# Kernel optimization log

Measured on AMD Instinct MI355X. Metric: run time of the kernel, lower is better.

The kernel has to match this reference:

```python
import jax, jax.numpy as jnp
import numpy as np

TAU = 2.0        # LIF membrane time constant
VTH = 1.0        # spike threshold
VRESET = 0.0     # hard reset voltage
ALPHA = 2.0      # ATan surrogate alpha
LN_EPS = 1e-5


@jax.custom_vjp
def atan_spike(x):
    # Heaviside forward, ATan surrogate backward (spikingjelly surrogate.ATan)
    return (x >= 0.0).astype(x.dtype)

def _atan_fwd(x):
    return atan_spike(x), x

def _atan_bwd(x, g):
    z = (jnp.pi / 2.0) * ALPHA * x
    return (g * (ALPHA / 2.0) / (1.0 + z * z),)

atan_spike.defvjp(_atan_fwd, _atan_bwd)


def layer_norm(x, w, b):
    mu = jnp.mean(x, axis=-1, keepdims=True)
    var = jnp.mean(jnp.square(x - mu), axis=-1, keepdims=True)
    return (x - mu) * jax.lax.rsqrt(var + LN_EPS) * w + b


def time_shift(x):
    # x: [B,T,C] -> x shifted by one step in time, zero-padded at t=0
    return jnp.pad(x, ((0, 0), (1, 0), (0, 0)))[:, :-1]


def wkv(time_decay, time_first, k, v):
    # Numerically-stable RWKV WKV recurrence. k, v: [B,T,C]
    w = -jnp.exp(time_decay)  # [C]
    u = time_first            # [C]
    B, T, C = k.shape
    kT = jnp.moveaxis(k, 1, 0)  # [T,B,C]
    vT = jnp.moveaxis(v, 1, 0)
    init = (jnp.zeros((B, C), k.dtype),
            jnp.zeros((B, C), k.dtype),
            jnp.full((B, C), -1e38, k.dtype))

    def step(carry, kv_t):
        aa, bb, pp = carry
        kt, vt = kv_t
        ww = u + kt
        p = jnp.maximum(pp, ww)
        e1 = jnp.exp(pp - p)
        e2 = jnp.exp(ww - p)
        y = (e1 * aa + e2 * vt) / (e1 * bb + e2)
        ww2 = pp + w
        p2 = jnp.maximum(ww2, kt)
        e1b = jnp.exp(ww2 - p2)
        e2b = jnp.exp(kt - p2)
        return (e1b * aa + e2b * vt, e1b * bb + e2b, p2), y

    _, yT = jax.lax.scan(step, init, (kT, vT))
    return jnp.moveaxis(yT, 0, 1)  # [B,T,C]


def lif(x):
    # MultiStepLIFNode: tau=2, decay_input=True, v_th=1, hard reset to 0.
    # Recurrence runs over the sequence dim (permute(1,0,2) in torch is layout only).
    xT = jnp.moveaxis(x, 1, 0)  # [T,B,C]
    v0 = jnp.zeros_like(xT[0])

    def step(v, xt):
        v = v + (xt - (v - VRESET)) / TAU
        s = atan_spike(v - VTH)
        v = (1.0 - s) * v + s * VRESET
        return v, s

    _, sT = jax.lax.scan(step, v0, xT)
    return jnp.moveaxis(sT, 0, 1)


def rwkv_time_mix(x, time_decay, time_first, mix_k, mix_v, mix_r, Wk, Wv, Wr, Wo):
    xx = time_shift(x)
    xk = x * mix_k + xx * (1.0 - mix_k)
    xv = x * mix_v + xx * (1.0 - mix_v)
    xr = x * mix_r + xx * (1.0 - mix_r)
    k = jnp.einsum('btc,cd->btd', xk, Wk)
    v = jnp.einsum('btc,cd->btd', xv, Wv)
    r = jax.nn.sigmoid(jnp.einsum('btc,cd->btd', xr, Wr))
    y = wkv(time_decay, time_first, k, v)
    return jnp.einsum('btc,cd->btd', r * y, Wo)


def rwkv_channel_mix(x, mix_k, mix_r, Wk, Wv, Wr):
    xx = time_shift(x)
    xk = x * mix_k + xx * (1.0 - mix_k)
    xr = x * mix_r + xx * (1.0 - mix_r)
    k = jnp.square(jax.nn.relu(jnp.einsum('btc,ch->bth', xk, Wk)))  # relu^2
    kv = jnp.einsum('bth,hc->btc', k, Wv)
    return jax.nn.sigmoid(jnp.einsum('btc,cd->btd', xr, Wr)) * kv


def setup_inputs() -> dict:
    key = jax.random.key(0)
    B, T, C, H = 8, 2048, 768, 3072
    ks = jax.random.split(key, 20)
    p = lambda k, shape, s=0.02: (jax.random.normal(k, shape, jnp.float32) * s)
    u = lambda k, shape: jax.random.uniform(k, shape, jnp.float32)
    return {
        'x': jax.random.normal(ks[0], (B, T, C), jnp.float32),
        'ln1_w': jnp.ones((C,), jnp.float32), 'ln1_b': jnp.zeros((C,), jnp.float32),
        'ln2_w': jnp.ones((C,), jnp.float32), 'ln2_b': jnp.zeros((C,), jnp.float32),
        'att_time_decay': p(ks[1], (C,), 1.0),
        'att_time_first': p(ks[2], (C,), 1.0),
        'att_mix_k': u(ks[3], (C,)), 'att_mix_v': u(ks[4], (C,)), 'att_mix_r': u(ks[5], (C,)),
        'att_Wk': p(ks[6], (C, C)), 'att_Wv': p(ks[7], (C, C)),
        'att_Wr': p(ks[8], (C, C)), 'att_Wo': p(ks[9], (C, C)),
        'ffn_mix_k': u(ks[10], (C,)), 'ffn_mix_r': u(ks[11], (C,)),
        'ffn_Wk': p(ks[12], (C, H)), 'ffn_Wv': p(ks[13], (H, C)), 'ffn_Wr': p(ks[14], (C, C)),
    }


def reference(x, ln1_w, ln1_b, ln2_w, ln2_b,
              att_time_decay, att_time_first, att_mix_k, att_mix_v, att_mix_r,
              att_Wk, att_Wv, att_Wr, att_Wo,
              ffn_mix_k, ffn_mix_r, ffn_Wk, ffn_Wv, ffn_Wr):
    # Block.forward with layer_id != 0 (no ln0, att path); dropout in eval mode.
    a = rwkv_time_mix(layer_norm(x, ln1_w, ln1_b), att_time_decay, att_time_first,
                      att_mix_k, att_mix_v, att_mix_r, att_Wk, att_Wv, att_Wr, att_Wo)
    x = x + lif(a)
    f = rwkv_channel_mix(layer_norm(x, ln2_w, ln2_b), ffn_mix_k, ffn_mix_r,
                         ffn_Wk, ffn_Wv, ffn_Wr)
    x = x + lif(f)
    return x
```

## Files before the change

kernel.cpp:

```cpp
#include <hip/hip_runtime.h>

#define B_ 8
#define T_ 2048
#define C_ 768
#define H_ 3072
#define BT_ (B_ * T_)
#define BC_ (B_ * C_)
#define WSEG 128
#define NWSEG 16
#define LSEG 128
#define NLSEG 16
#define LWARM 96

typedef unsigned short u16;
typedef short bf16x8 __attribute__((ext_vector_type(8)));
typedef float f32x4 __attribute__((ext_vector_type(4)));

__device__ __forceinline__ float b2f(u16 u) {
    union { unsigned i; float f; } w; w.i = ((unsigned)u) << 16; return w.f;
}
__device__ __forceinline__ u16 f2b(float f) {
    union { float f; unsigned i; } w; w.f = f;
    return (u16)((w.i + 0x7fffu + ((w.i >> 16) & 1u)) >> 16);
}

typedef __attribute__((address_space(3))) unsigned int lds_u32;
typedef const __attribute__((address_space(1))) unsigned int glb_u32;
__device__ __forceinline__ void gld_lds16(const void* g, void* l) {
    __builtin_amdgcn_global_load_lds((glb_u32*)g, (lds_u32*)l, 16, 0, 0);
}

template<int NOUT>
__global__ void lnmix(const float* __restrict__ x, const float* __restrict__ w,
                      const float* __restrict__ b,
                      const float* __restrict__ m1, const float* __restrict__ m2,
                      const float* __restrict__ m3,
                      u16* __restrict__ o1, u16* __restrict__ o2, u16* __restrict__ o3) {
    int row = blockIdx.x;
    int t = row % T_;
    const float* xr = x + (size_t)row * C_;
    const float* xp = xr - C_;
    int tid = threadIdx.x;
    float s = 0.f, s2 = 0.f, ps = 0.f, ps2 = 0.f;
    for (int i = tid; i < C_; i += 256) {
        float v = xr[i]; s += v; s2 += v * v;
        if (t > 0) { float u = xp[i]; ps += u; ps2 += u * u; }
    }
    for (int off = 32; off > 0; off >>= 1) {
        s += __shfl_down(s, off);  s2 += __shfl_down(s2, off);
        ps += __shfl_down(ps, off); ps2 += __shfl_down(ps2, off);
    }
    __shared__ float red[4][4];
    int wid = tid >> 6, lane = tid & 63;
    if (lane == 0) { red[wid][0] = s; red[wid][1] = s2; red[wid][2] = ps; red[wid][3] = ps2; }
    __syncthreads();
    if (tid == 0) {
        float a0 = 0, a1 = 0, a2 = 0, a3 = 0;
        for (int i = 0; i < 4; ++i) { a0 += red[i][0]; a1 += red[i][1]; a2 += red[i][2]; a3 += red[i][3]; }
        red[0][0] = a0; red[0][1] = a1; red[0][2] = a2; red[0][3] = a3;
    }
    __syncthreads();
    float mu = red[0][0] * (1.f / C_);
    float rs = rsqrtf(red[0][1] * (1.f / C_) - mu * mu + 1e-5f);
    float pmu = red[0][2] * (1.f / C_);
    float prs = rsqrtf(red[0][3] * (1.f / C_) - pmu * pmu + 1e-5f);
    size_t ob = (size_t)row * C_;
    for (int i = tid; i < C_; i += 256) {
        float wi = w[i], bi = b[i];
        float n = (xr[i] - mu) * rs * wi + bi;
        float np = (t > 0) ? (xp[i] - pmu) * prs * wi + bi : 0.f;
        o1[ob + i] = f2b(fmaf(m1[i], n - np, np));
        o2[ob + i] = f2b(fmaf(m2[i], n - np, np));
        if constexpr (NOUT == 3) o3[ob + i] = f2b(fmaf(m3[i], n - np, np));
    }
}

struct TCJ { const float* s; u16* d; int R, Ncol, nbx, b0; };
struct TC7 { TCJ j[7]; };
__global__ void tcast_all(TC7 jobs) {
    __shared__ float t[32][33];
    int bid = blockIdx.x;
    int ji = 0;
#pragma unroll
    for (int k = 1; k < 7; ++k) if (bid >= jobs.j[k].b0) ji = k;
    TCJ jb = jobs.j[ji];
    int local = bid - jb.b0;
    int bx = local % jb.nbx, by = local / jb.nbx;
    int c0 = bx * 32, r0 = by * 32;
    int col = threadIdx.x & 31, rw = threadIdx.x >> 5;
#pragma unroll
    for (int i = 0; i < 4; ++i) {
        int r = rw + i * 8;
        t[r][col] = jb.s[(size_t)(r0 + r) * jb.Ncol + c0 + col];
    }
    __syncthreads();
#pragma unroll
    for (int i = 0; i < 4; ++i) {
        int r = rw + i * 8;
        jb.d[(size_t)(c0 + r) * jb.R + r0 + col] = f2b(t[col][r]);
    }
}

__device__ __forceinline__ void gemm_core256(const u16* __restrict__ A,
                                             const u16* __restrict__ WT,
                                             int K, int m0, int n0,
                                             u16* L, f32x4 acc[8][4]) {
    const int tid = threadIdx.x;
    const int lane = tid & 63, wid = tid >> 6;
    const int wr = wid >> 2, wc = wid & 3;
    const int r16 = lane & 15, g = lane >> 4;

    const int srow = tid >> 3;
    const int sunit = tid & 7;
    const int ssw = sunit ^ (srow & 7);
    const u16* gA = A + (size_t)(m0 + srow) * K + ssw * 8;
    const u16* gB = WT + (size_t)(n0 + srow) * K + ssw * 8;
    u16* lA = L + tid * 8;
    u16* lB = L + 16384 + tid * 8;

#define STGA(buf) do { \
        gld_lds16(gA,                   lA + (buf) * 32768); \
        gld_lds16(gA + (size_t)64 * K,  lA + (buf) * 32768 + 4096); \
        gld_lds16(gA + (size_t)128 * K, lA + (buf) * 32768 + 8192); \
        gld_lds16(gA + (size_t)192 * K, lA + (buf) * 32768 + 12288); \
        gA += 64; } while (0)
#define STGB(buf) do { \
        gld_lds16(gB,                   lB + (buf) * 32768); \
        gld_lds16(gB + (size_t)64 * K,  lB + (buf) * 32768 + 4096); \
        gld_lds16(gB + (size_t)128 * K, lB + (buf) * 32768 + 8192); \
        gld_lds16(gB + (size_t)192 * K, lB + (buf) * 32768 + 12288); \
        gB += 64; } while (0)

    int offA[8], offB[4];
#pragma unroll
    for (int m = 0; m < 8; ++m) {
        int row = wr * 128 + m * 16 + r16;
        offA[m] = row * 64 + (g ^ (row & 7)) * 8;
    }
#pragma unroll
    for (int n = 0; n < 4; ++n) {
        int rob = wc * 64 + n * 16 + r16;
        offB[n] = 16384 + rob * 64 + (g ^ (rob & 7)) * 8;
    }

    const int nt = K >> 6;
    STGA(0); STGB(0);
    asm volatile("s_waitcnt vmcnt(0)" ::: "memory");
    __builtin_amdgcn_sched_barrier(0);
    __builtin_amdgcn_s_barrier();

    for (int t = 0; t < nt; ++t) {
        const u16* Lb = L + (t & 1) * 32768;
        const bool stg = (t + 1 < nt);
        bf16x8 a0[8], b0[4];
#pragma unroll
        for (int m = 0; m < 8; ++m) a0[m] = *(const bf16x8*)(Lb + offA[m]);
#pragma unroll
        for (int n = 0; n < 4; ++n) b0[n] = *(const bf16x8*)(Lb + offB[n]);
        __builtin_amdgcn_sched_barrier(0);
        if (stg) { STGA((t + 1) & 1); STGB((t + 1) & 1); }
        asm volatile("s_waitcnt lgkmcnt(0)" ::: "memory");
        __builtin_amdgcn_sched_barrier(0);
        __builtin_amdgcn_s_setprio(1);
#pragma unroll
        for (int m = 0; m < 8; ++m)
#pragma unroll
            for (int n = 0; n < 4; ++n)
                acc[m][n] = __builtin_amdgcn_mfma_f32_16x16x32_bf16(a0[m], b0[n], acc[m][n], 0, 0, 0);
        __builtin_amdgcn_s_setprio(0);
        __builtin_amdgcn_sched_barrier(0);
        bf16x8 a1[8], b1[4];
#pragma unroll
        for (int m = 0; m < 8; ++m) a1[m] = *(const bf16x8*)(Lb + (offA[m] ^ 32));
#pragma unroll
        for (int n = 0; n < 4; ++n) b1[n] = *(const bf16x8*)(Lb + (offB[n] ^ 32));
        asm volatile("s_waitcnt lgkmcnt(0)" ::: "memory");
        __builtin_amdgcn_sched_barrier(0);
        __builtin_amdgcn_s_setprio(1);
#pragma unroll
        for (int m = 0; m < 8; ++m)
#pragma unroll
            for (int n = 0; n < 4; ++n)
                acc[m][n] = __builtin_amdgcn_mfma_f32_16x16x32_bf16(a1[m], b1[n], acc[m][n], 0, 0, 0);
        __builtin_amdgcn_s_setprio(0);
        __builtin_amdgcn_sched_barrier(0);
        if (stg) {
            asm volatile("s_waitcnt vmcnt(0)" ::: "memory");
            __builtin_amdgcn_sched_barrier(0);
            __builtin_amdgcn_s_barrier();
        }
    }
#undef STGA
#undef STGB
}

__device__ __forceinline__ void xcd_remap2(int& bx, int& by) {
    const int gx = gridDim.x;
    const int nwg = gx * gridDim.y;
    const int lin = blockIdx.y * gx + blockIdx.x;
    const int q = nwg >> 3, r = nwg & 7;
    const int xcd = lin & 7, pos = lin >> 3;
    const int nid = (xcd < r ? xcd * (q + 1) : r * (q + 1) + (xcd - r) * q) + pos;
    const int g4 = gx << 2;
    const int grp = nid / g4, rem = nid - grp * g4;
    by = (grp << 2) + (rem & 3);
    bx = rem >> 2;
}

__device__ __forceinline__ void epilogue256(f32x4 acc[8][4], u16* O, const u16* Emul,
                                            int m0, int n0, int N, int mode, bool emul) {
    const int lane = threadIdx.x & 63, wid = threadIdx.x >> 6;
    const int wr = wid >> 2, wc = wid & 3;
    const int r16 = lane & 15, g = lane >> 4;
#pragma unroll
    for (int m = 0; m < 8; ++m)
#pragma unroll
        for (int n = 0; n < 4; ++n)
#pragma unroll
            for (int j = 0; j < 4; ++j) {
                int row = m0 + wr * 128 + m * 16 + g * 4 + j;
                int col = n0 + wc * 64 + n * 16 + r16;
                float v = acc[m][n][j];
                if (mode == 1) v = 1.f / (1.f + expf(-v));
                else if (mode == 2) { v = fmaxf(v, 0.f); v = v * v; }
                size_t o = (size_t)row * N + col;
                if (emul) v *= b2f(Emul[o]);
                O[o] = f2b(v);
            }
}

template<int MODE, bool EMUL>
__global__ __launch_bounds__(512, 1)
void gemm256(const u16* __restrict__ A, const u16* __restrict__ WT,
             u16* __restrict__ Cout, const u16* __restrict__ Emul, int N, int K) {
    __shared__ u16 L[65536];
    int bx, by;
    xcd_remap2(bx, by);
    const int m0 = by << 8, n0 = bx << 8;
    f32x4 acc[8][4];
#pragma unroll
    for (int i = 0; i < 8; ++i)
#pragma unroll
        for (int j = 0; j < 4; ++j)
#pragma unroll
            for (int q = 0; q < 4; ++q) acc[i][j][q] = 0.f;
    gemm_core256(A, WT, K, m0, n0, L, acc);
    epilogue256(acc, Cout, Emul, m0, n0, N, MODE, EMUL);
}

struct P3 {
    const u16 *A0, *A1, *A2;
    const u16 *W0, *W1, *W2;
    u16 *O0, *O1, *O2;
};
__global__ __launch_bounds__(512, 1)
void proj3(P3 p, int N, int K) {
    __shared__ u16 L[65536];
    const int z = blockIdx.z;
    const u16* A = (z == 0) ? p.A0 : (z == 1) ? p.A1 : p.A2;
    const u16* W = (z == 0) ? p.W0 : (z == 1) ? p.W1 : p.W2;
    u16* O = (z == 0) ? p.O0 : (z == 1) ? p.O1 : p.O2;
    int bx, by;
    xcd_remap2(bx, by);
    const int m0 = by << 8, n0 = bx << 8;
    f32x4 acc[8][4];
#pragma unroll
    for (int i = 0; i < 8; ++i)
#pragma unroll
        for (int j = 0; j < 4; ++j)
#pragma unroll
            for (int q = 0; q < 4; ++q) acc[i][j][q] = 0.f;
    gemm_core256(A, W, K, m0, n0, L, acc);
    epilogue256(acc, O, nullptr, m0, n0, N, (z == 2) ? 1 : 0, false);
}

struct J2 {
    const u16 *A0, *W0; u16 *O0;
    const u16 *A1, *W1; u16 *O1;
};
__global__ __launch_bounds__(512, 1)
void ffn1rr(J2 p, int K) {
    __shared__ u16 L[65536];
    int bx, by;
    xcd_remap2(bx, by);
    const bool isF = (bx < 12);
    const u16* A = isF ? p.A0 : p.A1;
    const u16* W = isF ? p.W0 : p.W1;
    u16* O = isF ? p.O0 : p.O1;
    const int N = isF ? 3072 : 768;
    const int m0 = by << 8;
    const int n0 = (isF ? bx : bx - 12) << 8;
    f32x4 acc[8][4];
#pragma unroll
    for (int i = 0; i < 8; ++i)
#pragma unroll
        for (int j = 0; j < 4; ++j)
#pragma unroll
            for (int q = 0; q < 4; ++q) acc[i][j][q] = 0.f;
    gemm_core256(A, W, K, m0, n0, L, acc);
    epilogue256(acc, O, nullptr, m0, n0, N, isF ? 2 : 1, false);
}

__global__ void wkv_p1(const float* __restrict__ td, const u16* __restrict__ K,
                       const u16* __restrict__ V, float* __restrict__ st) {
    int bc = blockIdx.x * 256 + threadIdx.x;
    int seg = blockIdx.y;
    int b = bc / C_, c = bc - b * C_;
    float w = -expf(td[c]);
    size_t off = (size_t)b * T_ * C_ + (size_t)seg * WSEG * C_ + c;
    float aa = 0.f, bb = 0.f, pp = -1e38f;
#pragma unroll 4
    for (int i = 0; i < WSEG; ++i) {
        float kt = b2f(K[off + (size_t)i * C_]);
        float vt = b2f(V[off + (size_t)i * C_]);
        float ww2 = pp + w;
        float p2 = fmaxf(ww2, kt);
        float e1 = expf(ww2 - p2);
        float e2 = expf(kt - p2);
        aa = e1 * aa + e2 * vt;
        bb = e1 * bb + e2;
        pp = p2;
    }
    int sidx = seg * 3 * BC_ + bc;
    st[sidx] = aa; st[sidx + BC_] = bb; st[sidx + 2 * BC_] = pp;
}

__global__ void wkv_p3(const float* __restrict__ td, const float* __restrict__ tf,
                       const u16* __restrict__ K, const u16* __restrict__ V,
                       const u16* __restrict__ R, const float* __restrict__ st,
                       u16* __restrict__ RY) {
    int bc = blockIdx.x * 256 + threadIdx.x;
    int seg = blockIdx.y;
    int b = bc / C_, c = bc - b * C_;
    float w = -expf(td[c]);
    float u = tf[c];
    float wL = w * (float)WSEG;
    float aa = 0.f, bb = 0.f, pp = -1e38f;
    for (int s = 0; s < seg; ++s) {
        int sidx = s * 3 * BC_ + bc;
        float la = st[sidx], lb = st[sidx + BC_], lp = st[sidx + 2 * BC_];
        float ppw = pp + wL;
        float p = fmaxf(ppw, lp);
        float e1 = expf(ppw - p), e2 = expf(lp - p);
        aa = e1 * aa + e2 * la;
        bb = e1 * bb + e2 * lb;
        pp = p;
    }
    size_t off = (size_t)b * T_ * C_ + (size_t)seg * WSEG * C_ + c;
#pragma unroll 4
    for (int i = 0; i < WSEG; ++i) {
        float kt = b2f(K[off + (size_t)i * C_]);
        float vt = b2f(V[off + (size_t)i * C_]);
        float rr = b2f(R[off + (size_t)i * C_]);
        float ww = u + kt;
        float p = fmaxf(pp, ww);
        float e1 = expf(pp - p);
        float e2 = expf(ww - p);
        RY[off + (size_t)i * C_] = f2b(rr * (e1 * aa + e2 * vt) / (e1 * bb + e2));
        float ww2 = pp + w;
        float p2 = fmaxf(ww2, kt);
        float e1b = expf(ww2 - p2);
        float e2b = expf(kt - p2);
        aa = e1b * aa + e2b * vt;
        bb = e1b * bb + e2b;
        pp = p2;
    }
}

__global__ void lif_add_b(const u16* __restrict__ cur, const float* __restrict__ base,
                          float* __restrict__ out) {
    int bc = blockIdx.x * 256 + threadIdx.x;
    int seg = blockIdx.y;
    int b = bc / C_, c = bc - b * C_;
    size_t rowbase = (size_t)b * T_ * C_ + c;
    int t0 = seg * LSEG;
    int tw = t0 - LWARM; if (tw < 0) tw = 0;
    int nw = t0 - tw;
    float v = 0.f;
    const u16* cp = cur + rowbase + (size_t)tw * C_;
#pragma unroll 8
    for (int i = 0; i < nw; ++i) {
        float xt = b2f(cp[(size_t)i * C_]);
        v += (xt - v) * 0.5f;
        v = (v >= 1.f) ? 0.f : v;
    }
    const u16* c2 = cur + rowbase + (size_t)t0 * C_;
    const float* bp = base + rowbase + (size_t)t0 * C_;
    float* op = out + rowbase + (size_t)t0 * C_;
#pragma unroll 8
    for (int i = 0; i < LSEG; ++i) {
        float xt = b2f(c2[(size_t)i * C_]);
        v += (xt - v) * 0.5f;
        float sp = (v >= 1.f) ? 1.f : 0.f;
        op[(size_t)i * C_] = bp[(size_t)i * C_] + sp;
        v = (sp > 0.f) ? 0.f : v;
    }
}

extern "C" void kernel_launch(void* const* d_in, const int* in_sizes, int n_in,
                              void* d_out, int out_size, void* d_ws, size_t ws_size,
                              hipStream_t stream) {
    const float* x    = (const float*)d_in[0];
    const float* ln1w = (const float*)d_in[1];
    const float* ln1b = (const float*)d_in[2];
    const float* ln2w = (const float*)d_in[3];
    const float* ln2b = (const float*)d_in[4];
    const float* td   = (const float*)d_in[5];
    const float* tf   = (const float*)d_in[6];
    const float* amk  = (const float*)d_in[7];
    const float* amv  = (const float*)d_in[8];
    const float* amr  = (const float*)d_in[9];
    const float* aWk  = (const float*)d_in[10];
    const float* aWv  = (const float*)d_in[11];
    const float* aWr  = (const float*)d_in[12];
    const float* aWo  = (const float*)d_in[13];
    const float* fmk  = (const float*)d_in[14];
    const float* fmr  = (const float*)d_in[15];
    const float* fWk  = (const float*)d_in[16];
    const float* fWv  = (const float*)d_in[17];
    const float* fWr  = (const float*)d_in[18];
    float* out = (float*)d_out;

    const size_t NBC = (size_t)BT_ * C_;
    u16* WkT = (u16*)d_ws;
    u16* WvT = WkT + 589824;
    u16* WrT = WvT + 589824;
    u16* WoT = WrT + 589824;
    u16* FrT = WoT + 589824;
    u16* FkT = FrT + 589824;
    u16* FvT = FkT + 2359296;
    float* st  = (float*)(FvT + 2359296);
    u16* S0 = (u16*)(st + NWSEG * 3 * BC_);
    u16* S1 = S0 + NBC;
    u16* S2 = S1 + NBC;
    u16* S3 = S2 + NBC;
    u16* Hbuf = S3 + NBC;
    size_t fixed_b = (size_t)((char*)Hbuf - (char*)d_ws);

    int NCH = 4;
    if (ws_size >= fixed_b + ((size_t)BT_ * H_ + NBC) * 2) NCH = 1;
    else if (ws_size >= fixed_b + ((size_t)(BT_ / 2) * H_ + NBC / 2) * 2) NCH = 2;
    const int CH = BT_ / NCH;
    u16* Fbuf = Hbuf + (size_t)CH * H_;

    u16* Kb = (u16*)d_out;
    u16* Vb = Kb + NBC;

    {
        TC7 jobs;
        const float* srcs[7] = {aWk, aWv, aWr, aWo, fWr, fWk, fWv};
        u16* dsts[7] = {WkT, WvT, WrT, WoT, FrT, FkT, FvT};
        int Rs[7]    = {768, 768, 768, 768, 768, 768, 3072};
        int Ns[7]    = {768, 768, 768, 768, 768, 3072, 768};
        int b0 = 0;
        for (int k = 0; k < 7; ++k) {
            jobs.j[k].s = srcs[k]; jobs.j[k].d = dsts[k];
            jobs.j[k].R = Rs[k]; jobs.j[k].Ncol = Ns[k];
            jobs.j[k].nbx = Ns[k] / 32; jobs.j[k].b0 = b0;
            b0 += (Ns[k] / 32) * (Rs[k] / 32);
        }
        tcast_all<<<b0, 256, 0, stream>>>(jobs);
    }

    lnmix<3><<<BT_, 256, 0, stream>>>(x, ln1w, ln1b, amk, amv, amr, S0, S1, S2);
    {
        P3 p{S0, S1, S2, WkT, WvT, WrT, Kb, Vb, S3};
        proj3<<<dim3(3, 64, 3), 512, 0, stream>>>(p, C_, C_);
    }
    wkv_p1<<<dim3(BC_ / 256, NWSEG), 256, 0, stream>>>(td, Kb, Vb, st);
    wkv_p3<<<dim3(BC_ / 256, NWSEG), 256, 0, stream>>>(td, tf, Kb, Vb, S3, st, S0);
    gemm256<0, false><<<dim3(3, 64), 512, 0, stream>>>(S0, WoT, S1, nullptr, C_, C_);
    lif_add_b<<<dim3(BC_ / 256, NLSEG), 256, 0, stream>>>(S1, x, out);
    lnmix<2><<<BT_, 256, 0, stream>>>(out, ln2w, ln2b, fmk, fmr, nullptr, S0, S1, nullptr);

    if (NCH == 1) {
        J2 p{S0, FkT, Hbuf, S1, FrT, S2};
        ffn1rr<<<dim3(15, 64), 512, 0, stream>>>(p, C_);
        gemm256<0, true><<<dim3(3, 64), 512, 0, stream>>>(Hbuf, FvT, Fbuf, S2, C_, H_);
        lif_add_b<<<dim3(BC_ / 256, NLSEG), 256, 0, stream>>>(Fbuf, out, out);
    } else {
        gemm256<1, false><<<dim3(3, 64), 512, 0, stream>>>(S1, FrT, S2, nullptr, C_, C_);
        for (int ch = 0; ch < NCH; ++ch) {
            const u16* xk2c = S0 + (size_t)ch * CH * C_;
            const u16* rrc  = S2 + (size_t)ch * CH * C_;
            gemm256<2, false><<<dim3(12, CH / 256), 512, 0, stream>>>(xk2c, FkT, Hbuf, nullptr, H_, C_);
            gemm256<0, true><<<dim3(3, CH / 256), 512, 0, stream>>>(Hbuf, FvT, Fbuf, rrc, C_, H_);
            lif_add_b<<<dim3((CH / T_) * C_ / 256, NLSEG), 256, 0, stream>>>(
                Fbuf, out + (size_t)ch * CH * C_, out + (size_t)ch * CH * C_);
        }
    }
}
```

Baseline: 563.9 us.

## Restructure 256x256 GEMM main loop into eight-phase quadrant ping-pong pipeline

```diff
diff --git a/kernel.cpp b/kernel.cpp
--- a/kernel.cpp
+++ b/kernel.cpp
@@ -112,86 +112,124 @@
 
     const int srow = tid >> 3;
     const int sunit = tid & 7;
-    const int ssw = sunit ^ (srow & 7);
-    const u16* gA = A + (size_t)(m0 + srow) * K + ssw * 8;
-    const u16* gB = WT + (size_t)(n0 + srow) * K + ssw * 8;
-    u16* lA = L + tid * 8;
-    u16* lB = L + 16384 + tid * 8;
-
-#define STGA(buf) do { \
-        gld_lds16(gA,                   lA + (buf) * 32768); \
-        gld_lds16(gA + (size_t)64 * K,  lA + (buf) * 32768 + 4096); \
-        gld_lds16(gA + (size_t)128 * K, lA + (buf) * 32768 + 8192); \
-        gld_lds16(gA + (size_t)192 * K, lA + (buf) * 32768 + 12288); \
-        gA += 64; } while (0)
-#define STGB(buf) do { \
-        gld_lds16(gB,                   lB + (buf) * 32768); \
-        gld_lds16(gB + (size_t)64 * K,  lB + (buf) * 32768 + 4096); \
-        gld_lds16(gB + (size_t)128 * K, lB + (buf) * 32768 + 8192); \
-        gld_lds16(gB + (size_t)192 * K, lB + (buf) * 32768 + 12288); \
-        gB += 64; } while (0)
+    const u16* pa = A + (size_t)(m0 + srow) * K + ((sunit ^ (srow & 7)) << 3);
+    const u16* pb = WT + (size_t)(n0 + srow) * K + ((sunit ^ (srow & 7)) << 3);
+    u16* lbase = L + tid * 8;
+
+#define STG_A(d, h) do { \
+        const u16* gp = pa + (size_t)((h) ? 128 : 0) * K; \
+        u16* lp = lbase + ((d) * 2 + (h)) * 8192; \
+        gld_lds16(gp, lp); gld_lds16(gp + (size_t)64 * K, lp + 4096); } while (0)
+#define STG_B(d, h) do { \
+        const u16* gp = pb + (size_t)((h) ? 128 : 0) * K; \
+        u16* lp = lbase + 32768 + ((d) * 2 + (h)) * 8192; \
+        gld_lds16(gp, lp); gld_lds16(gp + (size_t)64 * K, lp + 4096); } while (0)
 
     int offA[8], offB[4];
 #pragma unroll
     for (int m = 0; m < 8; ++m) {
-        int row = wr * 128 + m * 16 + r16;
-        offA[m] = row * 64 + (g ^ (row & 7)) * 8;
+        int lr = m * 16 + r16;
+        offA[m] = wr * 8192 + lr * 64 + ((g ^ (lr & 7)) << 3);
     }
 #pragma unroll
     for (int n = 0; n < 4; ++n) {
-        int rob = wc * 64 + n * 16 + r16;
-        offB[n] = 16384 + rob * 64 + (g ^ (rob & 7)) * 8;
-    }
+        int lrb = (wc & 1) * 64 + n * 16 + r16;
+        offB[n] = 32768 + (wc >> 1) * 8192 + lrb * 64 + ((g ^ (lrb & 7)) << 3);
+    }
+
+    bf16x8 aq[4][2], bq[2][2];
+
+#define RD_A(QM, DOFF) do { _Pragma("unroll") \
+        for (int mm = 0; mm < 4; ++mm) { \
+            int o = offA[(QM) * 4 + mm] + (DOFF); \
+            aq[mm][0] = *(const bf16x8*)(L + o); \
+            aq[mm][1] = *(const bf16x8*)(L + (o ^ 32)); } } while (0)
+#define RD_B(QN, DOFF) do { _Pragma("unroll") \
+        for (int nn = 0; nn < 2; ++nn) { \
+            int o = offB[(QN) * 2 + nn] + (DOFF); \
+            bq[nn][0] = *(const bf16x8*)(L + o); \
+            bq[nn][1] = *(const bf16x8*)(L + (o ^ 32)); } } while (0)
+#define MM16(QM, QN) do { _Pragma("unroll") \
+        for (int mm = 0; mm < 4; ++mm) { _Pragma("unroll") \
+            for (int nn = 0; nn < 2; ++nn) { \
+                acc[(QM)*4+mm][(QN)*2+nn] = __builtin_amdgcn_mfma_f32_16x16x32_bf16(aq[mm][0], bq[nn][0], acc[(QM)*4+mm][(QN)*2+nn], 0, 0, 0); \
+                acc[(QM)*4+mm][(QN)*2+nn] = __builtin_amdgcn_mfma_f32_16x16x32_bf16(aq[mm][1], bq[nn][1], acc[(QM)*4+mm][(QN)*2+nn], 0, 0, 0); } } } while (0)
+
+#define PH_MID(MMSTMT) \
+        __builtin_amdgcn_s_barrier(); \
+        asm volatile("s_waitcnt lgkmcnt(0)" ::: "memory"); \
+        __builtin_amdgcn_sched_barrier(0); \
+        __builtin_amdgcn_s_setprio(1); \
+        MMSTMT; \
+        __builtin_amdgcn_s_setprio(0); \
+        __builtin_amdgcn_sched_barrier(0);
 
     const int nt = K >> 6;
-    STGA(0); STGB(0);
-    asm volatile("s_waitcnt vmcnt(0)" ::: "memory");
+    const int nIter = nt >> 1;
+    STG_A(0, 0); STG_A(0, 1); pa += 64;
+    STG_B(0, 0); STG_B(0, 1); pb += 64;
+    STG_A(1, 0); STG_A(1, 1); pa += 64;
+    STG_B(1, 0);
+    asm volatile("s_waitcnt vmcnt(6)" ::: "memory");
     __builtin_amdgcn_sched_barrier(0);
     __builtin_amdgcn_s_barrier();
 
-    for (int t = 0; t < nt; ++t) {
-        const u16* Lb = L + (t & 1) * 32768;
-        const bool stg = (t + 1 < nt);
-        bf16x8 a0[8], b0[4];
-#pragma unroll
-        for (int m = 0; m < 8; ++m) a0[m] = *(const bf16x8*)(Lb + offA[m]);
-#pragma unroll
-        for (int n = 0; n < 4; ++n) b0[n] = *(const bf16x8*)(Lb + offB[n]);
-        __builtin_amdgcn_sched_barrier(0);
-        if (stg) { STGA((t + 1) & 1); STGB((t + 1) & 1); }
-        asm volatile("s_waitcnt lgkmcnt(0)" ::: "memory");
-        __builtin_amdgcn_sched_barrier(0);
-        __builtin_amdgcn_s_setprio(1);
-#pragma unroll
-        for (int m = 0; m < 8; ++m)
-#pragma unroll
-            for (int n = 0; n < 4; ++n)
-                acc[m][n] = __builtin_amdgcn_mfma_f32_16x16x32_bf16(a0[m], b0[n], acc[m][n], 0, 0, 0);
-        __builtin_amdgcn_s_setprio(0);
-        __builtin_amdgcn_sched_barrier(0);
-        bf16x8 a1[8], b1[4];
-#pragma unroll
-        for (int m = 0; m < 8; ++m) a1[m] = *(const bf16x8*)(Lb + (offA[m] ^ 32));
-#pragma unroll
-        for (int n = 0; n < 4; ++n) b1[n] = *(const bf16x8*)(Lb + (offB[n] ^ 32));
-        asm volatile("s_waitcnt lgkmcnt(0)" ::: "memory");
-        __builtin_amdgcn_sched_barrier(0);
-        __builtin_amdgcn_s_setprio(1);
-#pragma unroll
-        for (int m = 0; m < 8; ++m)
-#pragma unroll
-            for (int n = 0; n < 4; ++n)
-                acc[m][n] = __builtin_amdgcn_mfma_f32_16x16x32_bf16(a1[m], b1[n], acc[m][n], 0, 0, 0);
-        __builtin_amdgcn_s_setprio(0);
-        __builtin_amdgcn_sched_barrier(0);
-        if (stg) {
-            asm volatile("s_waitcnt vmcnt(0)" ::: "memory");
+    for (int i = 0; i < nIter; ++i) {
+        const bool last = (i == nIter - 1);
+        RD_A(0, 0); RD_B(0, 0);
+        __builtin_amdgcn_sched_barrier(0);
+        STG_B(1, 1); pb += 64;
+        PH_MID(MM16(0, 0));
+        __builtin_amdgcn_s_barrier();
+        RD_B(1, 0);
+        __builtin_amdgcn_sched_barrier(0);
+        if (!last) STG_A(0, 0);
+        PH_MID(MM16(0, 1));
+        __builtin_amdgcn_s_barrier();
+        RD_A(1, 0);
+        __builtin_amdgcn_sched_barrier(0);
+        if (!last) { STG_A(0, 1); pa += 64; }
+        PH_MID(MM16(1, 1));
+        __builtin_amdgcn_s_barrier();
+        RD_B(0, 0);
+        __builtin_amdgcn_sched_barrier(0);
+        if (!last) STG_B(0, 0);
+        PH_MID(MM16(1, 0));
+        if (last) asm volatile("s_waitcnt vmcnt(0)" ::: "memory");
+        else      asm volatile("s_waitcnt vmcnt(6)" ::: "memory");
+        __builtin_amdgcn_sched_barrier(0);
+        __builtin_amdgcn_s_barrier();
+        RD_A(0, 16384); RD_B(0, 16384);
+        __builtin_amdgcn_sched_barrier(0);
+        if (!last) { STG_B(0, 1); pb += 64; }
+        PH_MID(MM16(0, 0));
+        __builtin_amdgcn_s_barrier();
+        RD_B(1, 16384);
+        __builtin_amdgcn_sched_barrier(0);
+        if (!last) STG_A(1, 0);
+        PH_MID(MM16(0, 1));
+        __builtin_amdgcn_s_barrier();
+        RD_A(1, 16384);
+        __builtin_amdgcn_sched_barrier(0);
+        if (!last) { STG_A(1, 1); pa += 64; }
+        PH_MID(MM16(1, 1));
+        __builtin_amdgcn_s_barrier();
+        RD_B(0, 16384);
+        __builtin_amdgcn_sched_barrier(0);
+        if (!last) STG_B(1, 0);
+        PH_MID(MM16(1, 0));
+        if (!last) {
+            asm volatile("s_waitcnt vmcnt(6)" ::: "memory");
             __builtin_amdgcn_sched_barrier(0);
             __builtin_amdgcn_s_barrier();
         }
     }
-#undef STGA
-#undef STGB
+#undef STG_A
+#undef STG_B
+#undef RD_A
+#undef RD_B
+#undef MM16
+#undef PH_MID
 }
 
 __device__ __forceinline__ void xcd_remap2(int& bx, int& by) {
```

New measurement: 566.9 us. No clear change (+0.5%).

## Vectorize layernorm, WKV and LIF scans and shorten time segments

Applied to the files above, without the earlier changes.

```diff
diff --git a/kernel.cpp b/kernel.cpp
--- a/kernel.cpp
+++ b/kernel.cpp
@@ -6,10 +6,10 @@
 #define H_ 3072
 #define BT_ (B_ * T_)
 #define BC_ (B_ * C_)
-#define WSEG 128
-#define NWSEG 16
-#define LSEG 128
-#define NLSEG 16
+#define WSEG 64
+#define NWSEG 32
+#define LSEG 64
+#define NLSEG 32
 #define LWARM 96
 
 typedef unsigned short u16;
@@ -31,47 +31,85 @@
 }
 
 template<int NOUT>
-__global__ void lnmix(const float* __restrict__ x, const float* __restrict__ w,
-                      const float* __restrict__ b,
-                      const float* __restrict__ m1, const float* __restrict__ m2,
-                      const float* __restrict__ m3,
-                      u16* __restrict__ o1, u16* __restrict__ o2, u16* __restrict__ o3) {
-    int row = blockIdx.x;
-    int t = row % T_;
-    const float* xr = x + (size_t)row * C_;
-    const float* xp = xr - C_;
-    int tid = threadIdx.x;
+__global__ __launch_bounds__(512)
+void lnmixw(const float* __restrict__ x, const float* __restrict__ w,
+            const float* __restrict__ b,
+            const float* __restrict__ m1, const float* __restrict__ m2,
+            const float* __restrict__ m3,
+            u16* __restrict__ o1, u16* __restrict__ o2, u16* __restrict__ o3) {
+    const int wv = threadIdx.x >> 6, lane = threadIdx.x & 63;
+    const int row = blockIdx.x * 8 + wv;
+    const int t = row % T_;
+    const float4* xr4 = (const float4*)(x + (size_t)row * C_);
+    const float4* xp4 = (const float4*)(x + (size_t)(row - 1) * C_);
+    float4 c[3], p[3];
+#pragma unroll
+    for (int j = 0; j < 3; ++j) c[j] = xr4[lane + j * 64];
+    if (t > 0) {
+#pragma unroll
+        for (int j = 0; j < 3; ++j) p[j] = xp4[lane + j * 64];
+    } else {
+#pragma unroll
+        for (int j = 0; j < 3; ++j) p[j] = make_float4(0.f, 0.f, 0.f, 0.f);
+    }
     float s = 0.f, s2 = 0.f, ps = 0.f, ps2 = 0.f;
-    for (int i = tid; i < C_; i += 256) {
-        float v = xr[i]; s += v; s2 += v * v;
-        if (t > 0) { float u = xp[i]; ps += u; ps2 += u * u; }
-    }
+#pragma unroll
+    for (int j = 0; j < 3; ++j) {
+        s += c[j].x + c[j].y + c[j].z + c[j].w;
+        s2 += c[j].x * c[j].x + c[j].y * c[j].y + c[j].z * c[j].z + c[j].w * c[j].w;
+        ps += p[j].x + p[j].y + p[j].z + p[j].w;
+        ps2 += p[j].x * p[j].x + p[j].y * p[j].y + p[j].z * p[j].z + p[j].w * p[j].w;
+    }
+#pragma unroll
     for (int off = 32; off > 0; off >>= 1) {
         s += __shfl_down(s, off);  s2 += __shfl_down(s2, off);
         ps += __shfl_down(ps, off); ps2 += __shfl_down(ps2, off);
     }
-    __shared__ float red[4][4];
-    int wid = tid >> 6, lane = tid & 63;
-    if (lane == 0) { red[wid][0] = s; red[wid][1] = s2; red[wid][2] = ps; red[wid][3] = ps2; }
-    __syncthreads();
-    if (tid == 0) {
-        float a0 = 0, a1 = 0, a2 = 0, a3 = 0;
-        for (int i = 0; i < 4; ++i) { a0 += red[i][0]; a1 += red[i][1]; a2 += red[i][2]; a3 += red[i][3]; }
-        red[0][0] = a0; red[0][1] = a1; red[0][2] = a2; red[0][3] = a3;
-    }
-    __syncthreads();
-    float mu = red[0][0] * (1.f / C_);
-    float rs = rsqrtf(red[0][1] * (1.f / C_) - mu * mu + 1e-5f);
-    float pmu = red[0][2] * (1.f / C_);
-    float prs = rsqrtf(red[0][3] * (1.f / C_) - pmu * pmu + 1e-5f);
-    size_t ob = (size_t)row * C_;
-    for (int i = tid; i < C_; i += 256) {
-        float wi = w[i], bi = b[i];
-        float n = (xr[i] - mu) * rs * wi + bi;
-        float np = (t > 0) ? (xp[i] - pmu) * prs * wi + bi : 0.f;
-        o1[ob + i] = f2b(fmaf(m1[i], n - np, np));
-        o2[ob + i] = f2b(fmaf(m2[i], n - np, np));
-        if constexpr (NOUT == 3) o3[ob + i] = f2b(fmaf(m3[i], n - np, np));
+    s = __shfl(s, 0); s2 = __shfl(s2, 0); ps = __shfl(ps, 0); ps2 = __shfl(ps2, 0);
+    const float mu = s * (1.f / C_);
+    const float rs = rsqrtf(s2 * (1.f / C_) - mu * mu + 1e-5f);
+    const float pmu = ps * (1.f / C_);
+    const float prs = rsqrtf(ps2 * (1.f / C_) - pmu * pmu + 1e-5f);
+    const size_t ob = (size_t)row * C_;
+#pragma unroll
+    for (int j = 0; j < 3; ++j) {
+        int fi = lane + j * 64;
+        float4 w4 = ((const float4*)w)[fi];
+        float4 b4 = ((const float4*)b)[fi];
+        float4 n, np;
+        n.x = (c[j].x - mu) * rs * w4.x + b4.x;
+        n.y = (c[j].y - mu) * rs * w4.y + b4.y;
+        n.z = (c[j].z - mu) * rs * w4.z + b4.z;
+        n.w = (c[j].w - mu) * rs * w4.w + b4.w;
+        if (t > 0) {
+            np.x = (p[j].x - pmu) * prs * w4.x + b4.x;
+            np.y = (p[j].y - pmu) * prs * w4.y + b4.y;
+            np.z = (p[j].z - pmu) * prs * w4.z + b4.z;
+            np.w = (p[j].w - pmu) * prs * w4.w + b4.w;
+        } else {
+            np = make_float4(0.f, 0.f, 0.f, 0.f);
+        }
+        float4 mm = ((const float4*)m1)[fi];
+        ushort4 ov;
+        ov.x = f2b(fmaf(mm.x, n.x - np.x, np.x));
+        ov.y = f2b(fmaf(mm.y, n.y - np.y, np.y));
+        ov.z = f2b(fmaf(mm.z, n.z - np.z, np.z));
+        ov.w = f2b(fmaf(mm.w, n.w - np.w, np.w));
+        *(ushort4*)(o1 + ob + fi * 4) = ov;
+        mm = ((const float4*)m2)[fi];
+        ov.x = f2b(fmaf(mm.x, n.x - np.x, np.x));
+        ov.y = f2b(fmaf(mm.y, n.y - np.y, np.y));
+        ov.z = f2b(fmaf(mm.z, n.z - np.z, np.z));
+        ov.w = f2b(fmaf(mm.w, n.w - np.w, np.w));
+        *(ushort4*)(o2 + ob + fi * 4) = ov;
+        if constexpr (NOUT == 3) {
+            mm = ((const float4*)m3)[fi];
+            ov.x = f2b(fmaf(mm.x, n.x - np.x, np.x));
+            ov.y = f2b(fmaf(mm.y, n.y - np.y, np.y));
+            ov.z = f2b(fmaf(mm.z, n.z - np.z, np.z));
+            ov.w = f2b(fmaf(mm.w, n.w - np.w, np.w));
+            *(ushort4*)(o3 + ob + fi * 4) = ov;
+        }
     }
 }
 
@@ -303,97 +341,137 @@
 
 __global__ void wkv_p1(const float* __restrict__ td, const u16* __restrict__ K,
                        const u16* __restrict__ V, float* __restrict__ st) {
-    int bc = blockIdx.x * 256 + threadIdx.x;
+    int idx = blockIdx.x * 256 + threadIdx.x;
     int seg = blockIdx.y;
-    int b = bc / C_, c = bc - b * C_;
-    float w = -expf(td[c]);
+    int c2 = idx * 2;
+    int b = c2 / C_, c = c2 - b * C_;
+    float w0 = -expf(td[c]), w1 = -expf(td[c + 1]);
     size_t off = (size_t)b * T_ * C_ + (size_t)seg * WSEG * C_ + c;
-    float aa = 0.f, bb = 0.f, pp = -1e38f;
+    float aa0 = 0.f, bb0 = 0.f, pp0 = -1e38f;
+    float aa1 = 0.f, bb1 = 0.f, pp1 = -1e38f;
 #pragma unroll 4
     for (int i = 0; i < WSEG; ++i) {
-        float kt = b2f(K[off + (size_t)i * C_]);
-        float vt = b2f(V[off + (size_t)i * C_]);
-        float ww2 = pp + w;
-        float p2 = fmaxf(ww2, kt);
-        float e1 = expf(ww2 - p2);
-        float e2 = expf(kt - p2);
-        aa = e1 * aa + e2 * vt;
-        bb = e1 * bb + e2;
-        pp = p2;
-    }
-    int sidx = seg * 3 * BC_ + bc;
-    st[sidx] = aa; st[sidx + BC_] = bb; st[sidx + 2 * BC_] = pp;
+        ushort2 k2 = *(const ushort2*)(K + off + (size_t)i * C_);
+        ushort2 v2 = *(const ushort2*)(V + off + (size_t)i * C_);
+        {
+            float kt = b2f(k2.x), vt = b2f(v2.x);
+            float ww = pp0 + w0;
+            float p = fmaxf(ww, kt);
+            float e1 = expf(ww - p), e2 = expf(kt - p);
+            aa0 = e1 * aa0 + e2 * vt; bb0 = e1 * bb0 + e2; pp0 = p;
+        }
+        {
+            float kt = b2f(k2.y), vt = b2f(v2.y);
+            float ww = pp1 + w1;
+            float p = fmaxf(ww, kt);
+            float e1 = expf(ww - p), e2 = expf(kt - p);
+            aa1 = e1 * aa1 + e2 * vt; bb1 = e1 * bb1 + e2; pp1 = p;
+        }
+    }
+    int sidx = seg * 3 * BC_ + b * C_ + c;
+    *(float2*)(st + sidx) = make_float2(aa0, aa1);
+    *(float2*)(st + sidx + BC_) = make_float2(bb0, bb1);
+    *(float2*)(st + sidx + 2 * BC_) = make_float2(pp0, pp1);
 }
 
 __global__ void wkv_p3(const float* __restrict__ td, const float* __restrict__ tf,
                        const u16* __restrict__ K, const u16* __restrict__ V,
                        const u16* __restrict__ R, const float* __restrict__ st,
                        u16* __restrict__ RY) {
-    int bc = blockIdx.x * 256 + threadIdx.x;
+    int idx = blockIdx.x * 256 + threadIdx.x;
     int seg = blockIdx.y;
-    int b = bc / C_, c = bc - b * C_;
-    float w = -expf(td[c]);
-    float u = tf[c];
-    float wL = w * (float)WSEG;
-    float aa = 0.f, bb = 0.f, pp = -1e38f;
+    int c2 = idx * 2;
+    int b = c2 / C_, c = c2 - b * C_;
+    float w0 = -expf(td[c]), w1 = -expf(td[c + 1]);
+    float u0 = tf[c], u1 = tf[c + 1];
+    float wL0 = w0 * (float)WSEG, wL1 = w1 * (float)WSEG;
+    float aa0 = 0.f, bb0 = 0.f, pp0 = -1e38f;
+    float aa1 = 0.f, bb1 = 0.f, pp1 = -1e38f;
     for (int s = 0; s < seg; ++s) {
-        int sidx = s * 3 * BC_ + bc;
-        float la = st[sidx], lb = st[sidx + BC_], lp = st[sidx + 2 * BC_];
-        float ppw = pp + wL;
-        float p = fmaxf(ppw, lp);
-        float e1 = expf(ppw - p), e2 = expf(lp - p);
-        aa = e1 * aa + e2 * la;
-        bb = e1 * bb + e2 * lb;
-        pp = p;
+        int sidx = s * 3 * BC_ + b * C_ + c;
+        float2 la = *(const float2*)(st + sidx);
+        float2 lb = *(const float2*)(st + sidx + BC_);
+        float2 lp = *(const float2*)(st + sidx + 2 * BC_);
+        {
+            float ppw = pp0 + wL0;
+            float p = fmaxf(ppw, lp.x);
+            float e1 = expf(ppw - p), e2 = expf(lp.x - p);
+            aa0 = e1 * aa0 + e2 * la.x; bb0 = e1 * bb0 + e2 * lb.x; pp0 = p;
+        }
+        {
+            float ppw = pp1 + wL1;
+            float p = fmaxf(ppw, lp.y);
+            float e1 = expf(ppw - p), e2 = expf(lp.y - p);
+            aa1 = e1 * aa1 + e2 * la.y; bb1 = e1 * bb1 + e2 * lb.y; pp1 = p;
+        }
     }
     size_t off = (size_t)b * T_ * C_ + (size_t)seg * WSEG * C_ + c;
 #pragma unroll 4
     for (int i = 0; i < WSEG; ++i) {
-        float kt = b2f(K[off + (size_t)i * C_]);
-        float vt = b2f(V[off + (size_t)i * C_]);
-        float rr = b2f(R[off + (size_t)i * C_]);
-        float ww = u + kt;
-        float p = fmaxf(pp, ww);
-        float e1 = expf(pp - p);
-        float e2 = expf(ww - p);
-        RY[off + (size_t)i * C_] = f2b(rr * (e1 * aa + e2 * vt) / (e1 * bb + e2));
-        float ww2 = pp + w;
-        float p2 = fmaxf(ww2, kt);
-        float e1b = expf(ww2 - p2);
-        float e2b = expf(kt - p2);
-        aa = e1b * aa + e2b * vt;
-        bb = e1b * bb + e2b;
-        pp = p2;
+        ushort2 k2 = *(const ushort2*)(K + off + (size_t)i * C_);
+        ushort2 v2 = *(const ushort2*)(V + off + (size_t)i * C_);
+        ushort2 r2 = *(const ushort2*)(R + off + (size_t)i * C_);
+        ushort2 o2v;
+        {
+            float kt = b2f(k2.x), vt = b2f(v2.x), rr = b2f(r2.x);
+            float ww = u0 + kt;
+            float p = fmaxf(pp0, ww);
+            float e1 = expf(pp0 - p), e2 = expf(ww - p);
+            o2v.x = f2b(rr * (e1 * aa0 + e2 * vt) / (e1 * bb0 + e2));
+            float ww2 = pp0 + w0;
+            float p2 = fmaxf(ww2, kt);
+            float e1b = expf(ww2 - p2), e2b = expf(kt - p2);
+            aa0 = e1b * aa0 + e2b * vt; bb0 = e1b * bb0 + e2b; pp0 = p2;
+        }
+        {
+            float kt = b2f(k2.y), vt = b2f(v2.y), rr = b2f(r2.y);
+            float ww = u1 + kt;
+            float p = fmaxf(pp1, ww);
+            float e1 = expf(pp1 - p), e2 = expf(ww - p);
+            o2v.y = f2b(rr * (e1 * aa1 + e2 * vt) / (e1 * bb1 + e2));
+            float ww2 = pp1 + w1;
+            float p2 = fmaxf(ww2, kt);
+            float e1b = expf(ww2 - p2), e2b = expf(kt - p2);
+            aa1 = e1b * aa1 + e2b * vt; bb1 = e1b * bb1 + e2b; pp1 = p2;
+        }
+        *(ushort2*)(RY + off + (size_t)i * C_) = o2v;
     }
 }
 
 __global__ void lif_add_b(const u16* __restrict__ cur, const float* __restrict__ base,
                           float* __restrict__ out) {
-    int bc = blockIdx.x * 256 + threadIdx.x;
+    int idx = blockIdx.x * 256 + threadIdx.x;
     int seg = blockIdx.y;
-    int b = bc / C_, c = bc - b * C_;
+    int c2 = idx * 2;
+    int b = c2 / C_, c = c2 - b * C_;
     size_t rowbase = (size_t)b * T_ * C_ + c;
     int t0 = seg * LSEG;
     int tw = t0 - LWARM; if (tw < 0) tw = 0;
     int nw = t0 - tw;
-    float v = 0.f;
+    float v0 = 0.f, v1 = 0.f;
     const u16* cp = cur + rowbase + (size_t)tw * C_;
 #pragma unroll 8
     for (int i = 0; i < nw; ++i) {
-        float xt = b2f(cp[(size_t)i * C_]);
-        v += (xt - v) * 0.5f;
-        v = (v >= 1.f) ? 0.f : v;
-    }
-    const u16* c2 = cur + rowbase + (size_t)t0 * C_;
+        ushort2 x2 = *(const ushort2*)(cp + (size_t)i * C_);
+        v0 += (b2f(x2.x) - v0) * 0.5f;
+        v0 = (v0 >= 1.f) ? 0.f : v0;
+        v1 += (b2f(x2.y) - v1) * 0.5f;
+        v1 = (v1 >= 1.f) ? 0.f : v1;
+    }
+    const u16* cq = cur + rowbase + (size_t)t0 * C_;
     const float* bp = base + rowbase + (size_t)t0 * C_;
     float* op = out + rowbase + (size_t)t0 * C_;
 #pragma unroll 8
     for (int i = 0; i < LSEG; ++i) {
-        float xt = b2f(c2[(size_t)i * C_]);
-        v += (xt - v) * 0.5f;
-        float sp = (v >= 1.f) ? 1.f : 0.f;
-        op[(size_t)i * C_] = bp[(size_t)i * C_] + sp;
-        v = (sp > 0.f) ? 0.f : v;
+        ushort2 x2 = *(const ushort2*)(cq + (size_t)i * C_);
+        float2 b2 = *(const float2*)(bp + (size_t)i * C_);
+        v0 += (b2f(x2.x) - v0) * 0.5f;
+        float s0 = (v0 >= 1.f) ? 1.f : 0.f;
+        v1 += (b2f(x2.y) - v1) * 0.5f;
+        float s1 = (v1 >= 1.f) ? 1.f : 0.f;
+        *(float2*)(op + (size_t)i * C_) = make_float2(b2.x + s0, b2.y + s1);
+        v0 = (s0 > 0.f) ? 0.f : v0;
+        v1 = (s1 > 0.f) ? 0.f : v1;
     }
 }
 
@@ -462,22 +540,22 @@
         tcast_all<<<b0, 256, 0, stream>>>(jobs);
     }
 
-    lnmix<3><<<BT_, 256, 0, stream>>>(x, ln1w, ln1b, amk, amv, amr, S0, S1, S2);
+    lnmixw<3><<<BT_ / 8, 512, 0, stream>>>(x, ln1w, ln1b, amk, amv, amr, S0, S1, S2);
     {
         P3 p{S0, S1, S2, WkT, WvT, WrT, Kb, Vb, S3};
         proj3<<<dim3(3, 64, 3), 512, 0, stream>>>(p, C_, C_);
     }
-    wkv_p1<<<dim3(BC_ / 256, NWSEG), 256, 0, stream>>>(td, Kb, Vb, st);
-    wkv_p3<<<dim3(BC_ / 256, NWSEG), 256, 0, stream>>>(td, tf, Kb, Vb, S3, st, S0);
+    wkv_p1<<<dim3(BC_ / 512, NWSEG), 256, 0, stream>>>(td, Kb, Vb, st);
+    wkv_p3<<<dim3(BC_ / 512, NWSEG), 256, 0, stream>>>(td, tf, Kb, Vb, S3, st, S0);
     gemm256<0, false><<<dim3(3, 64), 512, 0, stream>>>(S0, WoT, S1, nullptr, C_, C_);
-    lif_add_b<<<dim3(BC_ / 256, NLSEG), 256, 0, stream>>>(S1, x, out);
-    lnmix<2><<<BT_, 256, 0, stream>>>(out, ln2w, ln2b, fmk, fmr, nullptr, S0, S1, nullptr);
+    lif_add_b<<<dim3(BC_ / 512, NLSEG), 256, 0, stream>>>(S1, x, out);
+    lnmixw<2><<<BT_ / 8, 512, 0, stream>>>(out, ln2w, ln2b, fmk, fmr, nullptr, S0, S1, nullptr);
 
     if (NCH == 1) {
         J2 p{S0, FkT, Hbuf, S1, FrT, S2};
         ffn1rr<<<dim3(15, 64), 512, 0, stream>>>(p, C_);
         gemm256<0, true><<<dim3(3, 64), 512, 0, stream>>>(Hbuf, FvT, Fbuf, S2, C_, H_);
-        lif_add_b<<<dim3(BC_ / 256, NLSEG), 256, 0, stream>>>(Fbuf, out, out);
+        lif_add_b<<<dim3(BC_ / 512, NLSEG), 256, 0, stream>>>(Fbuf, out, out);
     } else {
         gemm256<1, false><<<dim3(3, 64), 512, 0, stream>>>(S1, FrT, S2, nullptr, C_, C_);
         for (int ch = 0; ch < NCH; ++ch) {
@@ -485,7 +563,7 @@
             const u16* rrc  = S2 + (size_t)ch * CH * C_;
             gemm256<2, false><<<dim3(12, CH / 256), 512, 0, stream>>>(xk2c, FkT, Hbuf, nullptr, H_, C_);
             gemm256<0, true><<<dim3(3, CH / 256), 512, 0, stream>>>(Hbuf, FvT, Fbuf, rrc, C_, H_);
-            lif_add_b<<<dim3((CH / T_) * C_ / 256, NLSEG), 256, 0, stream>>>(
+            lif_add_b<<<dim3((CH / T_) * C_ / 512, NLSEG), 256, 0, stream>>>(
                 Fbuf, out + (size_t)ch * CH * C_, out + (size_t)ch * CH * C_);
         }
     }
```

New measurement: 529.9 us. -6.0%, faster.
